# Optimization experiments

Measured on AMD Instinct MI355X. Metric: run time of the kernel, lower is better.

Reference implementation:

```python
import jax, jax.numpy as jnp
import numpy as np

B, M, N, P, H = 8192, 4, 2, 2, 128
D5 = M * 5            # FC5 output = m * in_mult_KNet
D2H = (H + H) * 40    # FC2 hidden = d_input_FC2 * out_mult_KNet


def _lin(x, W, b):
    return x @ W.T + b


def _gru(x, h, Wih, Whh, bih, bhh):
    # PyTorch GRU cell math (single layer, single step)
    gi = x @ Wih.T + bih   # [B, 3H]
    gh = h @ Whh.T + bhh   # [B, 3H]
    ir, iz, inn = jnp.split(gi, 3, axis=-1)
    hr, hz, hn = jnp.split(gh, 3, axis=-1)
    r = jax.nn.sigmoid(ir + hr)
    z = jax.nn.sigmoid(iz + hz)
    n = jnp.tanh(inn + r * hn)
    return (1.0 - z) * n + z * h


def setup_inputs() -> dict:
    key = jax.random.key(0)
    ks = iter(jax.random.split(key, 64))
    rn = lambda *s: jax.random.normal(next(ks), s, dtype=jnp.float32)
    sc = lambda d: np.float32(1.0 / np.sqrt(d))
    inp = {
        'y': rn(B, N, 1), 'u': rn(B, P, 1), 'm1x_post': rn(B, M, 1),
        'h_Q': jnp.zeros((B, H), jnp.float32),
        'h_Sigma': jnp.zeros((B, H), jnp.float32),
        'h_S': jnp.zeros((B, H), jnp.float32),
        'F_mat': jnp.eye(M, dtype=jnp.float32) + 0.1 * rn(M, M),
        'G_mat': 0.1 * rn(M, P),
        'H_mat': 0.5 * rn(N, M),
        'innov_logit': jnp.float32(0.0),
        'W_fc5': rn(D5, M) * sc(M), 'b_fc5': rn(D5) * 0.01,
        'Wih_Q': rn(3 * H, D5) * sc(H), 'Whh_Q': rn(3 * H, H) * sc(H),
        'bih_Q': rn(3 * H) * 0.01, 'bhh_Q': rn(3 * H) * 0.01,
        'Wih_Sig': rn(3 * H, H) * sc(H), 'Whh_Sig': rn(3 * H, H) * sc(H),
        'bih_Sig': rn(3 * H) * 0.01, 'bhh_Sig': rn(3 * H) * 0.01,
        'W_fc1': rn(N * N, H) * sc(H), 'b_fc1': rn(N * N) * 0.01,
        'W_fc7': rn(N, N) * sc(N), 'b_fc7': rn(N) * 0.01,
        'Wih_S': rn(3 * H, N * N + N) * sc(H), 'Whh_S': rn(3 * H, H) * sc(H),
        'bih_S': rn(3 * H) * 0.01, 'bhh_S': rn(3 * H) * 0.01,
        'W_fc2a': rn(D2H, 2 * H) * sc(2 * H), 'b_fc2a': rn(D2H) * 0.01,
        'W_fc2b': rn(N * M, D2H) * sc(D2H), 'b_fc2b': rn(N * M) * 0.01,
        'W_fc3': rn(M * M, H + N * M) * sc(H + N * M), 'b_fc3': rn(M * M) * 0.01,
        'W_fc4': rn(H, H + M * M) * sc(H + M * M), 'b_fc4': rn(H) * 0.01,
    }
    return inp


def reference(y, u, m1x_post, h_Q, h_Sigma, h_S, F_mat, G_mat, H_mat, innov_logit,
              W_fc5, b_fc5, Wih_Q, Whh_Q, bih_Q, bhh_Q,
              Wih_Sig, Whh_Sig, bih_Sig, bhh_Sig,
              W_fc1, b_fc1, W_fc7, b_fc7,
              Wih_S, Whh_S, bih_S, bhh_S,
              W_fc2a, b_fc2a, W_fc2b, b_fc2b,
              W_fc3, b_fc3, W_fc4, b_fc4):
    relu = jax.nn.relu
    # --- step_prior: linear system model f(x,u)=Fx+Gu, h(x)=Hx (no normalization) ---
    x_post = m1x_post[..., 0]                      # [B, M]
    x_prior = x_post @ F_mat.T + u[..., 0] @ G_mat.T
    y_pred = x_prior @ H_mat.T                     # [B, N]
    dy = y[..., 0] - y_pred                        # innovation [B, N]
    # --- KGain_step (dropout = identity at inference) ---
    out5 = relu(_lin(x_prior, W_fc5, b_fc5))       # [B, 20]
    hQ_new = _gru(out5, h_Q, Wih_Q, Whh_Q, bih_Q, bhh_Q)
    hSig = _gru(hQ_new, h_Sigma, Wih_Sig, Whh_Sig, bih_Sig, bhh_Sig)
    out1 = relu(_lin(hSig, W_fc1, b_fc1))          # [B, n^2]
    out7 = relu(_lin(dy, W_fc7, b_fc7))            # [B, n]
    hS_new = _gru(jnp.concatenate([out1, out7], -1), h_S, Wih_S, Whh_S, bih_S, bhh_S)
    in2 = jnp.concatenate([hSig, hS_new], -1)      # [B, 256]
    out2 = _lin(relu(_lin(in2, W_fc2a, b_fc2a)), W_fc2b, b_fc2b)  # KG flat [B, n*m]
    out3 = relu(_lin(jnp.concatenate([hS_new, out2], -1), W_fc3, b_fc3))
    hSig_new = relu(_lin(jnp.concatenate([hSig, out3], -1), W_fc4, b_fc4))
    # --- posterior update ---
    KG = out2.reshape(B, M, N)
    gamma = jax.nn.sigmoid(innov_logit)
    inov = gamma * jnp.einsum('bmn,bn->bm', KG, dy)
    m1x_posterior = (x_prior + inov)[..., None]    # [B, M, 1]
    return m1x_posterior, hQ_new, hSig_new, hS_new
```

## Files before the change

kernel.cpp:

```cpp
#include <hip/hip_runtime.h>
#include <hip/hip_bf16.h>

typedef __attribute__((ext_vector_type(8))) short bf16x8;
typedef __attribute__((ext_vector_type(4))) float f32x4;
typedef __attribute__((ext_vector_type(4))) short s16x4;
typedef __attribute__((ext_vector_type(4))) float f32v4;
typedef unsigned short u16;

__device__ inline u16 f2b(float f){ __hip_bfloat16 b = __float2bfloat16(f); return __builtin_bit_cast(unsigned short, b); }
__device__ inline float b2f(u16 u){ unsigned int x = ((unsigned int)u)<<16; return __builtin_bit_cast(float, x); }
__device__ inline float sigm(float x){ return 1.f/(1.f+__expf(-x)); }
__device__ inline float tanhfast(float x){ float e = __expf(2.f*x); return 1.f - 2.f/(e+1.f); }

__device__ inline f32x4 mfma16(bf16x8 a, bf16x8 b, f32x4 c){
  return __builtin_amdgcn_mfma_f32_16x16x32_bf16(a, b, c, 0, 0, 0);
}

struct CVA {
  const float *w2a, *w2b, *wihQ, *whhQ, *wihSg, *whhSg, *wihS, *whhS, *wfc3, *wfc4;
  u16 *waB, *wbB, *wihQp, *whhQb, *wihSgB, *whhSgB, *wihSp, *whhSb, *wfc3p, *wfc4p;
};

__global__ __launch_bounds__(256) void kconv(CVA a){
  int id = blockIdx.x*256 + threadIdx.x;
  if (id < 2621440){
    int t  = id >> 12;
    int r  = id & 4095;
    int kk = r >> 9;
    int l  = (r >> 3) & 63;
    int e  = id & 7;
    int col = t*16 + (l & 15);
    int k   = kk*32 + (l >> 4)*8 + e;
    a.waB[id] = f2b(a.w2a[col*256 + k]);
    return;
  }
  id -= 2621440;
  if (id < 163840){
    int s = id >> 9;
    int r = id & 511;
    int l = r >> 3;
    int e = r & 7;
    int o = l & 15;
    int k = s*32 + (l >> 4)*8 + e;
    a.wbB[id] = (o < 8) ? f2b(a.w2b[o*10240 + k]) : (u16)0;
    return;
  }
  id -= 163840;
  if (id < 12288){ int j=id>>5, k=id&31; a.wihQp[id] = (k<20)? f2b(a.wihQ[j*20+k]) : (u16)0; return; }
  id -= 12288;
  if (id < 49152){ a.whhQb[id] = f2b(a.whhQ[id]); return; }
  id -= 49152;
  if (id < 49152){ a.wihSgB[id] = f2b(a.wihSg[id]); return; }
  id -= 49152;
  if (id < 49152){ a.whhSgB[id] = f2b(a.whhSg[id]); return; }
  id -= 49152;
  if (id < 12288){ int j=id>>5, k=id&31; a.wihSp[id] = (k<6)? f2b(a.wihS[j*6+k]) : (u16)0; return; }
  id -= 12288;
  if (id < 49152){ a.whhSb[id] = f2b(a.whhS[id]); return; }
  id -= 49152;
  if (id < 2560){ int j=id/160, k=id%160; a.wfc3p[id] = (k<136)? f2b(a.wfc3[j*136+k]) : (u16)0; return; }
  id -= 2560;
  if (id < 20480){ int j=id/160, k=id%160; a.wfc4p[id] = (k<144)? f2b(a.wfc4[j*144+k]) : (u16)0; return; }
}

template<int KX, int LDX, bool SOUT, bool GB16, bool GF32>
__device__ __forceinline__ void gru_step(
    const u16* sX, const u16* sH,
    const u16* __restrict__ Wih, const int ldwih, const u16* __restrict__ Whh,
    const float* __restrict__ bih, const float* __restrict__ bhh,
    float* __restrict__ gOutF, u16* sOut, u16* __restrict__ gB16)
{
  const int tid = threadIdx.x;
  const int w = tid>>6, lane = tid&63, c = lane&15, khi = lane>>4;
  for (int nn=0; nn<2; ++nn){
    const int n = w*2+nn;
    const int j = n*16 + c;
    const float bir=bih[j], biz=bih[128+j], bin=bih[256+j];
    const float bhr=bhh[j], bhz=bhh[128+j], bhn=bhh[256+j];
    bf16x8 BX0[KX], BX1[KX], BX2[KX], BH0[4], BH1[4], BH2[4];
    #pragma unroll
    for (int kk=0;kk<KX;++kk){
      const u16* p = Wih + j*ldwih + kk*32 + khi*8;
      BX0[kk] = *(const bf16x8*)(p);
      BX1[kk] = *(const bf16x8*)(p + 128*ldwih);
      BX2[kk] = *(const bf16x8*)(p + 256*ldwih);
    }
    #pragma unroll
    for (int kk=0;kk<4;++kk){
      const u16* p = Whh + j*128 + kk*32 + khi*8;
      BH0[kk] = *(const bf16x8*)(p);
      BH1[kk] = *(const bf16x8*)(p + 128*128);
      BH2[kk] = *(const bf16x8*)(p + 256*128);
    }
    #pragma unroll
    for (int m=0;m<2;++m){
      f32x4 ir={0,0,0,0}, iz={0,0,0,0}, inx={0,0,0,0};
      f32x4 hr={0,0,0,0}, hz={0,0,0,0}, hn={0,0,0,0};
      #pragma unroll
      for (int kk=0;kk<KX;++kk){
        bf16x8 A = *(const bf16x8*)(sX + (m*16+c)*LDX + kk*32 + khi*8);
        ir  = mfma16(A, BX0[kk], ir);
        iz  = mfma16(A, BX1[kk], iz);
        inx = mfma16(A, BX2[kk], inx);
      }
      #pragma unroll
      for (int kk=0;kk<4;++kk){
        bf16x8 A = *(const bf16x8*)(sH + (m*16+c)*136 + kk*32 + khi*8);
        hr = mfma16(A, BH0[kk], hr);
        hz = mfma16(A, BH1[kk], hz);
        hn = mfma16(A, BH2[kk], hn);
      }
      #pragma unroll
      for (int e=0;e<4;++e){
        int r = m*16 + khi*4 + e;
        float rg = sigm(ir[e]+hr[e]+bir+bhr);
        float zg = sigm(iz[e]+hz[e]+biz+bhz);
        float ng = tanhfast(inx[e]+bin + rg*(hn[e]+bhn));
        float hold = b2f(sH[r*136 + j]);
        float hv = (1.f-zg)*ng + zg*hold;
        if (GF32) gOutF[r*128 + j] = hv;
        if (SOUT) sOut[r*136 + j] = f2b(hv);
        if (GB16) gB16[r*256 + j] = f2b(hv);
      }
    }
  }
}

struct K1A {
  const float *y,*u,*m1x,*hQ,*hSg,*hS,*F,*G,*Hm,*W5,*b5,
              *bihQ,*bhhQ,*bihSg,*bhhSg,*W1,*b1,*W7,*b7,*bihS,*bhhS;
  const u16 *wihQp,*whhQ,*wihSg,*whhSg,*wihSp,*whhS;
  float *outHQ,*outHS,*xp,*dy;
  u16 *in2;
};

__device__ __forceinline__ void load_h_tile(u16* dst, const float* src, int row0){
  const int tid = threadIdx.x;
  #pragma unroll
  for (int i=0;i<4;++i){
    int f4 = tid + i*256;
    int r = f4>>5, c4 = f4&31;
    f32v4 v = *(const f32v4*)(src + (row0+r)*128 + c4*4);
    s16x4 o;
    o[0]=(short)f2b(v[0]); o[1]=(short)f2b(v[1]);
    o[2]=(short)f2b(v[2]); o[3]=(short)f2b(v[3]);
    *(s16x4*)(dst + r*136 + c4*4) = o;
  }
}

__global__ __launch_bounds__(256) void k1(K1A a){
  __shared__ u16 sX[32*40];
  __shared__ u16 sH[32*136];
  __shared__ u16 sXL[32*136];
  __shared__ u16 sSig[32*136];
  __shared__ float sDY[64];
  const int row0 = blockIdx.x*32;
  const int tid = threadIdx.x;

  load_h_tile(sH, a.hQ, row0);
  if (tid < 32){
    int r = tid, row = row0 + r;
    float xpost[4], uu[2], xpr[4];
    #pragma unroll
    for (int i=0;i<4;++i) xpost[i]=a.m1x[row*4+i];
    uu[0]=a.u[row*2]; uu[1]=a.u[row*2+1];
    #pragma unroll
    for (int i=0;i<4;++i){
      float s=0.f;
      #pragma unroll
      for (int jj=0;jj<4;++jj) s += a.F[i*4+jj]*xpost[jj];
      #pragma unroll
      for (int jj=0;jj<2;++jj) s += a.G[i*2+jj]*uu[jj];
      xpr[i]=s; a.xp[row*4+i]=s;
    }
    #pragma unroll
    for (int nn2=0;nn2<2;++nn2){
      float s=0.f;
      #pragma unroll
      for (int jj=0;jj<4;++jj) s += a.Hm[nn2*4+jj]*xpr[jj];
      float d = a.y[row*2+nn2]-s;
      a.dy[row*2+nn2]=d; sDY[r*2+nn2]=d;
    }
    #pragma unroll
    for (int o=0;o<20;++o){
      float s=a.b5[o];
      #pragma unroll
      for (int k=0;k<4;++k) s += a.W5[o*4+k]*xpr[k];
      sX[r*40+o]=f2b(fmaxf(s,0.f));
    }
    for (int o=20;o<40;++o) sX[r*40+o]=0;
  }
  __syncthreads();
  gru_step<1,40,true,false,true>(sX, sH, a.wihQp, 32, a.whhQ, a.bihQ, a.bhhQ,
                                 a.outHQ + row0*128, sXL, nullptr);
  __syncthreads();
  load_h_tile(sH, a.hSg, row0);
  __syncthreads();
  gru_step<4,136,true,true,false>(sXL, sH, a.wihSg, 128, a.whhSg, a.bihSg, a.bhhSg,
                                  nullptr, sSig, a.in2 + row0*256);
  __syncthreads();
  if (tid < 128){
    int r = tid>>2, o = tid&3;
    float s = a.b1[o];
    for (int k=0;k<128;++k) s += a.W1[o*128+k]*b2f(sSig[r*136+k]);
    sX[r*40+o] = f2b(fmaxf(s,0.f));
  } else if (tid < 192){
    int t = tid-128; int r=t>>1, o=t&1;
    float s = a.b7[o] + a.W7[o*2]*sDY[r*2] + a.W7[o*2+1]*sDY[r*2+1];
    sX[r*40+4+o] = f2b(fmaxf(s,0.f));
  }
  for (int i=tid;i<32*26;i+=256){ int r=i/26, cc=6+(i%26); sX[r*40+cc]=0; }
  load_h_tile(sH, a.hS, row0);
  __syncthreads();
  gru_step<1,40,false,true,true>(sX, sH, a.wihSp, 32, a.whhS, a.bihS, a.bhhS,
                                 a.outHS + row0*128, nullptr, a.in2 + row0*256 + 128);
}

struct K2A {
  const u16 *waB, *wbB, *in2;
  const float *b2a;
  float *parts;
};

__global__ __launch_bounds__(512) void k2(K2A a){
  __shared__ u16 sA[64*256];
  __shared__ u16 sHid[8*64*36];
  const int bid = blockIdx.x;
  const int rb = bid>>3, ch = bid&7;
  const int row0 = rb*64;
  const int tid = threadIdx.x;
  const int wid = tid>>6, lane = tid&63, c = lane&15, khi = lane>>4;

  #pragma unroll
  for (int i=0;i<8;++i){
    int idx = tid + i*512;
    int r = idx>>6, c4 = idx&63;
    s16x4 v = *(const s16x4*)(a.in2 + (size_t)(row0+r)*256 + c4*4);
    *(s16x4*)(sA + r*256 + ((c4*4) ^ ((r&7)<<3))) = v;
  }
  __syncthreads();

  u16* sHw = sHid + wid*2304;
  f32x4 C2[4];
  #pragma unroll
  for (int m=0;m<4;++m) C2[m] = (f32x4){0,0,0,0};

  for (int it=0; it<5; ++it){
    const int colb = ch*1280 + it*256 + wid*32;
    const int t0 = colb>>4;
    bf16x8 Bf[2][8];
    #pragma unroll
    for (int n2=0;n2<2;++n2)
      #pragma unroll
      for (int kk=0;kk<8;++kk)
        Bf[n2][kk] = *(const bf16x8*)(a.waB + (size_t)((t0+n2)*8+kk)*512 + lane*8);
    bf16x8 B2 = *(const bf16x8*)(a.wbB + (size_t)(colb>>5)*512 + lane*8);
    const float bias0 = a.b2a[colb + c];
    const float bias1 = a.b2a[colb + 16 + c];
    #pragma unroll
    for (int m=0;m<4;++m){
      const int row = m*16 + c;
      bf16x8 Af[8];
      #pragma unroll
      for (int kk=0;kk<8;++kk)
        Af[kk] = *(const bf16x8*)(sA + row*256 + ((kk*32 + khi*8) ^ ((row&7)<<3)));
      f32x4 c0={0,0,0,0}, c1={0,0,0,0};
      #pragma unroll
      for (int kk=0;kk<8;++kk){
        c0 = mfma16(Af[kk], Bf[0][kk], c0);
        c1 = mfma16(Af[kk], Bf[1][kk], c1);
      }
      #pragma unroll
      for (int e=0;e<4;++e){
        int rr = m*16 + khi*4 + e;
        sHw[rr*36 + c]      = f2b(fmaxf(c0[e]+bias0, 0.f));
        sHw[rr*36 + 16 + c] = f2b(fmaxf(c1[e]+bias1, 0.f));
      }
      bf16x8 A2 = *(const bf16x8*)(sHw + (m*16+c)*36 + khi*8);
      C2[m] = mfma16(A2, B2, C2[m]);
    }
  }
  __syncthreads();
  float* sRed = (float*)sHid;
  if (c < 8){
    #pragma unroll
    for (int m=0;m<4;++m)
      #pragma unroll
      for (int e=0;e<4;++e)
        sRed[wid*512 + (m*16+khi*4+e)*8 + c] = C2[m][e];
  }
  __syncthreads();
  {
    int i = tid;
    int r = i>>3, o = i&7;
    float s = 0.f;
    #pragma unroll
    for (int wv=0;wv<8;++wv) s += sRed[wv*512 + r*8 + o];
    a.parts[(size_t)ch*65536 + (size_t)(row0+r)*8 + o] = s;
  }
}

struct K3A {
  const float *parts;
  const float *b2b, *bfc3, *bfc4, *xp, *dy, *innov;
  const u16 *in2, *wfc3p, *wfc4p;
  float *outPost, *outHSig;
};

__global__ __launch_bounds__(256) void k3(K3A a){
  __shared__ u16 sA[64*168];
  __shared__ u16 sX4[64*168];
  __shared__ float sOut2[64*8];
  const int row0 = blockIdx.x*64;
  const int tid = threadIdx.x;
  for (int i=tid;i<512;i+=256){
    int r=i>>3, o=i&7, row=row0+r;
    float s = a.b2b[o];
    #pragma unroll
    for (int chv=0;chv<8;++chv) s += a.parts[chv*65536 + row*8 + o];
    sOut2[i]=s;
    sA[r*168+128+o]=f2b(s);
  }
  for (int i=tid;i<2048;i+=256){
    int r=i>>5, c4=i&31;
    *(s16x4*)(sA  + r*168 + c4*4) = *(const s16x4*)(a.in2 + (row0+r)*256 + 128 + c4*4);
    *(s16x4*)(sX4 + r*168 + c4*4) = *(const s16x4*)(a.in2 + (row0+r)*256 + c4*4);
  }
  for (int i=tid;i<64*6;i+=256){
    int r=i/6, c4=i%6;
    *(s16x4*)(sA + r*168 + 136 + c4*4) = (s16x4){0,0,0,0};
  }
  for (int i=tid;i<64*4;i+=256){
    int r=i>>2, c4=i&3;
    *(s16x4*)(sX4 + r*168 + 144 + c4*4) = (s16x4){0,0,0,0};
  }
  __syncthreads();
  {
    int r = tid>>2, m = tid&3, row = row0+r;
    float g = 1.f/(1.f+__expf(-a.innov[0]));
    float d0 = a.dy[row*2], d1 = a.dy[row*2+1];
    float k0 = sOut2[r*8+m*2], k1 = sOut2[r*8+m*2+1];
    a.outPost[row*4+m] = a.xp[row*4+m] + g*(k0*d0+k1*d1);
  }
  const int w = tid>>6, lane = tid&63, c = lane&15, khi = lane>>4;
  {
    f32x4 C3 = {0,0,0,0};
    #pragma unroll
    for (int kk=0;kk<5;++kk){
      bf16x8 A  = *(const bf16x8*)(sA + (w*16+c)*168 + kk*32 + khi*8);
      bf16x8 Bf = *(const bf16x8*)(a.wfc3p + c*160 + kk*32 + khi*8);
      C3 = mfma16(A,Bf,C3);
    }
    float bj = a.bfc3[c];
    #pragma unroll
    for (int e=0;e<4;++e){
      int r = w*16 + khi*4 + e;
      sX4[r*168 + 128 + c] = f2b(fmaxf(C3[e]+bj, 0.f));
    }
  }
  __syncthreads();
  for (int nn=0;nn<2;++nn){
    int j = (w*2+nn)*16 + c;
    bf16x8 Bf[5];
    #pragma unroll
    for (int kk=0;kk<5;++kk) Bf[kk] = *(const bf16x8*)(a.wfc4p + j*160 + kk*32 + khi*8);
    float bj = a.bfc4[j];
    #pragma unroll
    for (int m=0;m<4;++m){
      f32x4 C = {0,0,0,0};
      #pragma unroll
      for (int kk=0;kk<5;++kk){
        bf16x8 A = *(const bf16x8*)(sX4 + (m*16+c)*168 + kk*32 + khi*8);
        C = mfma16(A, Bf[kk], C);
      }
      #pragma unroll
      for (int e=0;e<4;++e){
        int r = m*16 + khi*4 + e;
        a.outHSig[(row0+r)*128 + j] = fmaxf(C[e]+bj, 0.f);
      }
    }
  }
}

extern "C" void kernel_launch(void* const* d_in, const int* in_sizes, int n_in,
                              void* d_out, int out_size, void* d_ws, size_t ws_size,
                              hipStream_t stream){
  const float* y    = (const float*)d_in[0];
  const float* u    = (const float*)d_in[1];
  const float* m1x  = (const float*)d_in[2];
  const float* hQ   = (const float*)d_in[3];
  const float* hSg  = (const float*)d_in[4];
  const float* hS   = (const float*)d_in[5];
  const float* F    = (const float*)d_in[6];
  const float* G    = (const float*)d_in[7];
  const float* Hm   = (const float*)d_in[8];
  const float* innov= (const float*)d_in[9];
  const float* W5   = (const float*)d_in[10];
  const float* b5   = (const float*)d_in[11];
  const float* WihQ = (const float*)d_in[12];
  const float* WhhQ = (const float*)d_in[13];
  const float* bihQ = (const float*)d_in[14];
  const float* bhhQ = (const float*)d_in[15];
  const float* WihSg= (const float*)d_in[16];
  const float* WhhSg= (const float*)d_in[17];
  const float* bihSg= (const float*)d_in[18];
  const float* bhhSg= (const float*)d_in[19];
  const float* W1   = (const float*)d_in[20];
  const float* b1   = (const float*)d_in[21];
  const float* W7   = (const float*)d_in[22];
  const float* b7   = (const float*)d_in[23];
  const float* WihS = (const float*)d_in[24];
  const float* WhhS = (const float*)d_in[25];
  const float* bihS = (const float*)d_in[26];
  const float* bhhS = (const float*)d_in[27];
  const float* W2a  = (const float*)d_in[28];
  const float* b2a  = (const float*)d_in[29];
  const float* W2b  = (const float*)d_in[30];
  const float* b2b  = (const float*)d_in[31];
  const float* W3   = (const float*)d_in[32];
  const float* b3   = (const float*)d_in[33];
  const float* W4   = (const float*)d_in[34];
  const float* b4   = (const float*)d_in[35];

  const size_t WS_NEEDED = 12547072;
  if (ws_size < WS_NEEDED) return;

  char* ws = (char*)d_ws;
  u16*  waB   = (u16*)(ws + 0);
  u16*  wbB   = (u16*)(ws + 5242880);
  u16*  in2B  = (u16*)(ws + 5570560);
  float* parts= (float*)(ws + 9764864);
  float* xp   = (float*)(ws + 11862016);
  float* dyb  = (float*)(ws + 11993088);
  u16* wihQp  = (u16*)(ws + 12058624);
  u16* whhQb  = (u16*)(ws + 12083200);
  u16* wihSgB = (u16*)(ws + 12181504);
  u16* whhSgB = (u16*)(ws + 12279808);
  u16* wihSp  = (u16*)(ws + 12378112);
  u16* whhSb  = (u16*)(ws + 12402688);
  u16* wfc3p  = (u16*)(ws + 12500992);
  u16* wfc4p  = (u16*)(ws + 12506112);

  float* outF    = (float*)d_out;
  float* outPost = outF;
  float* outHQ   = outF + 32768;
  float* outHSig = outF + 32768 + 1048576;
  float* outHS   = outF + 32768 + 2*1048576;

  CVA cv{W2a, W2b, WihQ, WhhQ, WihSg, WhhSg, WihS, WhhS, W3, W4,
         waB, wbB, wihQp, whhQb, wihSgB, whhSgB, wihSp, whhSb, wfc3p, wfc4p};
  kconv<<<dim3(11834), dim3(256), 0, stream>>>(cv);

  K1A a1{y,u,m1x,hQ,hSg,hS,F,G,Hm,W5,b5,bihQ,bhhQ,bihSg,bhhSg,W1,b1,W7,b7,bihS,bhhS,
         wihQp,whhQb,wihSgB,whhSgB,wihSp,whhSb,
         outHQ,outHS,xp,dyb,in2B};
  k1<<<dim3(256), dim3(256), 0, stream>>>(a1);

  K2A a2{waB, wbB, in2B, b2a, parts};
  k2<<<dim3(1024), dim3(512), 0, stream>>>(a2);

  K3A a3{parts, b2b, b3, b4, xp, dyb, innov, in2B, wfc3p, wfc4p, outPost, outHSig};
  k3<<<dim3(128), dim3(256), 0, stream>>>(a3);
}
```

Measured before the change: 108.1 us.

## Store in2 in MFMA fragment layout and enlarge k2 row tiles to reuse weights

Result: slower. 266.5 us (+146.5%).

```diff
diff --git a/kernel.cpp b/kernel.cpp
--- a/kernel.cpp
+++ b/kernel.cpp
@@ -14,6 +14,15 @@
 
 __device__ inline f32x4 mfma16(bf16x8 a, bf16x8 b, f32x4 c){
   return __builtin_amdgcn_mfma_f32_16x16x32_bf16(a, b, c, 0, 0, 0);
+}
+
+__device__ __forceinline__ void in2t_store(u16* t, int row, int col, u16 v){
+  int rt = row>>4, kk = col>>5, khi = (col>>3)&3, e = col&7;
+  t[(rt*8+kk)*512 + (khi*16 + (row&15))*8 + e] = v;
+}
+__device__ __forceinline__ s16x4 in2t_load4(const u16* t, int row, int col){
+  int rt = row>>4, kk = col>>5, khi = (col>>3)&3, e = col&7;
+  return *(const s16x4*)(t + (rt*8+kk)*512 + (khi*16 + (row&15))*8 + e);
 }
 
 struct CVA {
@@ -68,7 +77,8 @@
     const u16* sX, const u16* sH,
     const u16* __restrict__ Wih, const int ldwih, const u16* __restrict__ Whh,
     const float* __restrict__ bih, const float* __restrict__ bhh,
-    float* __restrict__ gOutF, u16* sOut, u16* __restrict__ gB16)
+    float* __restrict__ gOutF, u16* sOut,
+    u16* __restrict__ in2T, int row0, int colOff)
 {
   const int tid = threadIdx.x;
   const int w = tid>>6, lane = tid&63, c = lane&15, khi = lane>>4;
@@ -120,7 +130,7 @@
         float hv = (1.f-zg)*ng + zg*hold;
         if (GF32) gOutF[r*128 + j] = hv;
         if (SOUT) sOut[r*136 + j] = f2b(hv);
-        if (GB16) gB16[r*256 + j] = f2b(hv);
+        if (GB16) in2t_store(in2T, row0 + r, colOff + j, f2b(hv));
       }
     }
   }
@@ -131,7 +141,7 @@
               *bihQ,*bhhQ,*bihSg,*bhhSg,*W1,*b1,*W7,*b7,*bihS,*bhhS;
   const u16 *wihQp,*whhQ,*wihSg,*whhSg,*wihSp,*whhS;
   float *outHQ,*outHS,*xp,*dy;
-  u16 *in2;
+  u16 *in2T;
 };
 
 __device__ __forceinline__ void load_h_tile(u16* dst, const float* src, int row0){
@@ -192,12 +202,12 @@
   }
   __syncthreads();
   gru_step<1,40,true,false,true>(sX, sH, a.wihQp, 32, a.whhQ, a.bihQ, a.bhhQ,
-                                 a.outHQ + row0*128, sXL, nullptr);
+                                 a.outHQ + row0*128, sXL, nullptr, 0, 0);
   __syncthreads();
   load_h_tile(sH, a.hSg, row0);
   __syncthreads();
   gru_step<4,136,true,true,false>(sXL, sH, a.wihSg, 128, a.whhSg, a.bihSg, a.bhhSg,
-                                  nullptr, sSig, a.in2 + row0*256);
+                                  nullptr, sSig, a.in2T, row0, 0);
   __syncthreads();
   if (tid < 128){
     int r = tid>>2, o = tid&3;
@@ -213,40 +223,29 @@
   load_h_tile(sH, a.hS, row0);
   __syncthreads();
   gru_step<1,40,false,true,true>(sX, sH, a.wihSp, 32, a.whhS, a.bihS, a.bhhS,
-                                 a.outHS + row0*128, nullptr, a.in2 + row0*256 + 128);
+                                 a.outHS + row0*128, nullptr, a.in2T, row0, 128);
 }
 
 struct K2A {
-  const u16 *waB, *wbB, *in2;
+  const u16 *waB, *wbB, *in2T;
   const float *b2a;
   float *parts;
 };
 
 __global__ __launch_bounds__(512) void k2(K2A a){
-  __shared__ u16 sA[64*256];
-  __shared__ u16 sHid[8*64*36];
+  __shared__ u16 sHw[8][576];
+  __shared__ float sRed[8][256][8];
   const int bid = blockIdx.x;
-  const int rb = bid>>3, ch = bid&7;
-  const int row0 = rb*64;
+  const int rg = bid>>3, ch = bid&7;
   const int tid = threadIdx.x;
   const int wid = tid>>6, lane = tid&63, c = lane&15, khi = lane>>4;
 
+  f32x4 C2[16];
   #pragma unroll
-  for (int i=0;i<8;++i){
-    int idx = tid + i*512;
-    int r = idx>>6, c4 = idx&63;
-    s16x4 v = *(const s16x4*)(a.in2 + (size_t)(row0+r)*256 + c4*4);
-    *(s16x4*)(sA + r*256 + ((c4*4) ^ ((r&7)<<3))) = v;
-  }
-  __syncthreads();
-
-  u16* sHw = sHid + wid*2304;
-  f32x4 C2[4];
-  #pragma unroll
-  for (int m=0;m<4;++m) C2[m] = (f32x4){0,0,0,0};
-
-  for (int it=0; it<5; ++it){
-    const int colb = ch*1280 + it*256 + wid*32;
+  for (int i=0;i<16;++i) C2[i] = (f32x4){0,0,0,0};
+
+  for (int p=0; p<5; ++p){
+    const int colb = ch*1280 + p*256 + wid*32;
     const int t0 = colb>>4;
     bf16x8 Bf[2][8];
     #pragma unroll
@@ -258,52 +257,60 @@
     const float bias0 = a.b2a[colb + c];
     const float bias1 = a.b2a[colb + 16 + c];
     #pragma unroll
-    for (int m=0;m<4;++m){
-      const int row = m*16 + c;
-      bf16x8 Af[8];
-      #pragma unroll
-      for (int kk=0;kk<8;++kk)
-        Af[kk] = *(const bf16x8*)(sA + row*256 + ((kk*32 + khi*8) ^ ((row&7)<<3)));
-      f32x4 c0={0,0,0,0}, c1={0,0,0,0};
-      #pragma unroll
-      for (int kk=0;kk<8;++kk){
-        c0 = mfma16(Af[kk], Bf[0][kk], c0);
-        c1 = mfma16(Af[kk], Bf[1][kk], c1);
-      }
-      #pragma unroll
-      for (int e=0;e<4;++e){
-        int rr = m*16 + khi*4 + e;
-        sHw[rr*36 + c]      = f2b(fmaxf(c0[e]+bias0, 0.f));
-        sHw[rr*36 + 16 + c] = f2b(fmaxf(c1[e]+bias1, 0.f));
-      }
-      bf16x8 A2 = *(const bf16x8*)(sHw + (m*16+c)*36 + khi*8);
-      C2[m] = mfma16(A2, B2, C2[m]);
-    }
-  }
-  __syncthreads();
-  float* sRed = (float*)sHid;
+    for (int t=0;t<4;++t){
+      __syncthreads();
+      const int rtb = rg*16 + t*4;
+      #pragma unroll
+      for (int mh=0;mh<2;++mh){
+        bf16x8 Af[2][8];
+        #pragma unroll
+        for (int m2=0;m2<2;++m2)
+          #pragma unroll
+          for (int kk=0;kk<8;++kk)
+            Af[m2][kk] = *(const bf16x8*)(a.in2T + (size_t)((rtb + mh*2 + m2)*8 + kk)*512 + lane*8);
+        #pragma unroll
+        for (int m2=0;m2<2;++m2){
+          f32x4 c0={0,0,0,0}, c1={0,0,0,0};
+          #pragma unroll
+          for (int kk=0;kk<8;++kk){
+            c0 = mfma16(Af[m2][kk], Bf[0][kk], c0);
+            c1 = mfma16(Af[m2][kk], Bf[1][kk], c1);
+          }
+          #pragma unroll
+          for (int e=0;e<4;++e){
+            int rr = khi*4 + e;
+            sHw[wid][rr*36 + c]      = f2b(fmaxf(c0[e]+bias0, 0.f));
+            sHw[wid][rr*36 + 16 + c] = f2b(fmaxf(c1[e]+bias1, 0.f));
+          }
+          bf16x8 A2 = *(const bf16x8*)(&sHw[wid][c*36 + khi*8]);
+          C2[t*4 + mh*2 + m2] = mfma16(A2, B2, C2[t*4 + mh*2 + m2]);
+        }
+      }
+    }
+  }
   if (c < 8){
     #pragma unroll
-    for (int m=0;m<4;++m)
-      #pragma unroll
-      for (int e=0;e<4;++e)
-        sRed[wid*512 + (m*16+khi*4+e)*8 + c] = C2[m][e];
-  }
-  __syncthreads();
-  {
-    int i = tid;
-    int r = i>>3, o = i&7;
-    float s = 0.f;
-    #pragma unroll
-    for (int wv=0;wv<8;++wv) s += sRed[wv*512 + r*8 + o];
-    a.parts[(size_t)ch*65536 + (size_t)(row0+r)*8 + o] = s;
+    for (int t=0;t<4;++t)
+      #pragma unroll
+      for (int m=0;m<4;++m)
+        #pragma unroll
+        for (int e=0;e<4;++e)
+          sRed[wid][t*64 + m*16 + khi*4 + e][c] = C2[t*4+m][e];
+  }
+  __syncthreads();
+  for (int i=tid;i<2048;i+=512){
+    int r=i>>3, o=i&7;
+    float s=0.f;
+    #pragma unroll
+    for (int w=0;w<8;++w) s += sRed[w][r][o];
+    a.parts[(size_t)ch*65536 + (size_t)(rg*256+r)*8 + o] = s;
   }
 }
 
 struct K3A {
   const float *parts;
   const float *b2b, *bfc3, *bfc4, *xp, *dy, *innov;
-  const u16 *in2, *wfc3p, *wfc4p;
+  const u16 *in2T, *wfc3p, *wfc4p;
   float *outPost, *outHSig;
 };
 
@@ -323,8 +330,9 @@
   }
   for (int i=tid;i<2048;i+=256){
     int r=i>>5, c4=i&31;
-    *(s16x4*)(sA  + r*168 + c4*4) = *(const s16x4*)(a.in2 + (row0+r)*256 + 128 + c4*4);
-    *(s16x4*)(sX4 + r*168 + c4*4) = *(const s16x4*)(a.in2 + (row0+r)*256 + c4*4);
+    int row = row0 + r, col = c4*4;
+    *(s16x4*)(sX4 + r*168 + col) = in2t_load4(a.in2T, row, col);
+    *(s16x4*)(sA  + r*168 + col) = in2t_load4(a.in2T, row, 128 + col);
   }
   for (int i=tid;i<64*6;i+=256){
     int r=i/6, c4=i%6;
@@ -428,7 +436,7 @@
   char* ws = (char*)d_ws;
   u16*  waB   = (u16*)(ws + 0);
   u16*  wbB   = (u16*)(ws + 5242880);
-  u16*  in2B  = (u16*)(ws + 5570560);
+  u16*  in2T  = (u16*)(ws + 5570560);
   float* parts= (float*)(ws + 9764864);
   float* xp   = (float*)(ws + 11862016);
   float* dyb  = (float*)(ws + 11993088);
@@ -453,12 +461,12 @@
 
   K1A a1{y,u,m1x,hQ,hSg,hS,F,G,Hm,W5,b5,bihQ,bhhQ,bihSg,bhhSg,W1,b1,W7,b7,bihS,bhhS,
          wihQp,whhQb,wihSgB,whhSgB,wihSp,whhSb,
-         outHQ,outHS,xp,dyb,in2B};
+         outHQ,outHS,xp,dyb,in2T};
   k1<<<dim3(256), dim3(256), 0, stream>>>(a1);
 
-  K2A a2{waB, wbB, in2B, b2a, parts};
-  k2<<<dim3(1024), dim3(512), 0, stream>>>(a2);
-
-  K3A a3{parts, b2b, b3, b4, xp, dyb, innov, in2B, wfc3p, wfc4p, outPost, outHSig};
+  K2A a2{waB, wbB, in2T, b2a, parts};
+  k2<<<dim3(256), dim3(512), 0, stream>>>(a2);
+
+  K3A a3{parts, b2b, b3, b4, xp, dyb, innov, in2T, wfc3p, wfc4p, outPost, outHSig};
   k3<<<dim3(128), dim3(256), 0, stream>>>(a3);
 }
```
